# Kernel tuning notes

Measured on AMD Instinct MI355X. Metric: run time of the kernel, lower is better.

## Reference

```python
import jax, jax.numpy as jnp
import numpy as np

D_MODEL = 1024


def setup_inputs() -> dict:
    key = jax.random.key(0)
    k1, k2, k3, k4, k5, k6 = jax.random.split(key, 6)
    B, S, D = 4, 4096, D_MODEL
    scale = 1.0 / np.sqrt(D)
    return {
        "hidden": jax.random.normal(k1, (B, S, D), dtype=jnp.float32),
        "pre_emb": jax.random.normal(k2, (B, S, D), dtype=jnp.float32),
        "w1": jax.random.normal(k3, (D, D), dtype=jnp.float32) * scale,  # [in, out]
        "b1": jax.random.normal(k4, (D,), dtype=jnp.float32) * 0.01,
        "w2": jax.random.normal(k5, (D, D), dtype=jnp.float32) * scale,
        "b2": jax.random.normal(k6, (D,), dtype=jnp.float32) * 0.01,
    }


def reference(hidden, pre_emb, w1, b1, w2, b2):
    # h = Linear1(hidden); i = Linear2(hidden + pre_emb)
    h = jnp.einsum("bsd,de->bse", hidden, w1) + b1            # [B,S,D]
    i = jnp.einsum("bsd,de->bse", hidden + pre_emb, w2) + b2  # [B,S,D]
    attn = jnp.einsum("bqd,bkd->bqk", h, i)                   # [B,S,S]
    return jax.nn.softmax(attn, axis=-1)
```

## Files before the change

### kernel.cpp

```cpp
#include <hip/hip_runtime.h>
#include <hip/hip_bf16.h>
#include <stdint.h>

#define DM   1024
#define BATCH 4
#define SEQ  4096
#define MTOT (BATCH*SEQ)

typedef __attribute__((ext_vector_type(8))) short bf16x8;
typedef __attribute__((ext_vector_type(4))) float f32x4;

#define GLOAD_LDS16(gp, lp) __builtin_amdgcn_global_load_lds( \
    (const __attribute__((address_space(1))) unsigned int*)(gp), \
    (__attribute__((address_space(3))) unsigned int*)(lp), 16, 0, 0)

__device__ __forceinline__ ushort f2bf(float f){
  uint u = __float_as_uint(f);
  u += 0x7FFFu + ((u >> 16) & 1u);
  return (ushort)(u >> 16);
}
__device__ __forceinline__ float bf2f(ushort b){ return __uint_as_float(((uint)b) << 16); }

__device__ __forceinline__ void split4(const float4 v, ushort4& h4, ushort4& l4){
  h4.x = f2bf(v.x); l4.x = f2bf(v.x - bf2f(h4.x));
  h4.y = f2bf(v.y); l4.y = f2bf(v.y - bf2f(h4.y));
  h4.z = f2bf(v.z); l4.z = f2bf(v.z - bf2f(h4.z));
  h4.w = f2bf(v.w); l4.w = f2bf(v.w - bf2f(h4.w));
}

__global__ __launch_bounds__(256)
void prep_w_split(const float* __restrict__ w1, const float* __restrict__ w2,
                  ushort* __restrict__ w1h, ushort* __restrict__ w1l,
                  ushort* __restrict__ w2h, ushort* __restrict__ w2l){
  const float* w = blockIdx.y ? w2 : w1;
  ushort* oh = blockIdx.y ? w2h : w1h;
  ushort* ol = blockIdx.y ? w2l : w1l;
  size_t off = ((size_t)blockIdx.x * 256 + threadIdx.x) * 4;
  float4 v = *(const float4*)&w[off];
  ushort4 h4, l4; split4(v, h4, l4);
  *(ushort4*)&oh[off] = h4;
  *(ushort4*)&ol[off] = l4;
}

__global__ __launch_bounds__(256)
void prep_xy(const float* __restrict__ hidden, const float* __restrict__ pre,
             ushort* __restrict__ xh, ushort* __restrict__ xl,
             ushort* __restrict__ yh, ushort* __restrict__ yl,
             const float* __restrict__ c2, float* __restrict__ beta, int writeX){
  __shared__ float red[4];
  const int tid = threadIdx.x, lane = tid & 63, wid = tid >> 6;
  size_t off = ((size_t)blockIdx.x * 256 + tid) * 4;
  float4 h = *(const float4*)&hidden[off];
  float4 p = *(const float4*)&pre[off];
  float4 y = {h.x + p.x, h.y + p.y, h.z + p.z, h.w + p.w};
  ushort4 a, b;
  if (writeX){
    split4(h, a, b);
    *(ushort4*)&xh[off] = a;
    *(ushort4*)&xl[off] = b;
  }
  split4(y, a, b);
  *(ushort4*)&yh[off] = a;
  *(ushort4*)&yl[off] = b;

  float4 c = *(const float4*)&c2[tid * 4];
  float s = y.x * c.x + y.y * c.y + y.z * c.z + y.w * c.w;
  #pragma unroll
  for (int o = 32; o > 0; o >>= 1) s += __shfl_xor(s, o, 64);
  if (lane == 0) red[wid] = s;
  __syncthreads();
  if (tid == 0) beta[blockIdx.x] = red[0] + red[1] + red[2] + red[3];
}

__global__ __launch_bounds__(256)
void c2k(const float* __restrict__ w2, const float* __restrict__ b1,
         float* __restrict__ c2){
  const int wid = threadIdx.x >> 6, lane = threadIdx.x & 63;
  const int row = blockIdx.x * 4 + wid;
  float s = 0.f;
  #pragma unroll
  for (int t = 0; t < 16; t++){
    int e = lane + 64 * t;
    s += w2[(size_t)row * DM + e] * b1[e];
  }
  #pragma unroll
  for (int o = 32; o > 0; o >>= 1) s += __shfl_xor(s, o, 64);
  if (lane == 0) c2[row] = s;
}

__device__ __forceinline__ void bt_mainloop(
    const ushort* __restrict__ Aph, const ushort* __restrict__ Apl,
    const ushort* __restrict__ Bph, const ushort* __restrict__ Bpl,
    int m0, int n0, f32x4 (&acc)[4][4]){
  __shared__ alignas(16) ushort Ah[128*32];
  __shared__ alignas(16) ushort Al[128*32];
  __shared__ alignas(16) ushort Bh[128*32];
  __shared__ alignas(16) ushort Bl[128*32];

  const int tid = threadIdx.x;
  const int lane = tid & 63, wid = tid >> 6;
  const int wm = (wid & 1) * 64, wn = (wid >> 1) * 64;
  const int lr = lane & 15;
  const int lks = (((lane >> 4) ^ ((lane >> 1) & 3)) << 3);

  const ushort* plane = (wid == 0) ? Aph : (wid == 1) ? Apl : (wid == 2) ? Bph : Bpl;
  ushort* lds = (wid == 0) ? Ah : (wid == 1) ? Al : (wid == 2) ? Bh : Bl;
  const int r0 = (wid < 2) ? m0 : n0;
  const size_t goff = (size_t)(r0 + (lane >> 2)) * DM
                    + (size_t)(((lane & 3) ^ ((lane >> 3) & 3)) * 8);

  for (int k0 = 0; k0 < DM; k0 += 32){
    __syncthreads();
    const ushort* gp = plane + goff + k0;
    #pragma unroll
    for (int t = 0; t < 8; t++){
      GLOAD_LDS16(gp + (size_t)t * 16 * DM, lds + t * 512);
    }
    __syncthreads();

    bf16x8 fah[4], fal[4], fbh[4], fbl[4];
    #pragma unroll
    for (int i = 0; i < 4; i++){
      fah[i] = *(const bf16x8*)&Ah[(wm + i*16 + lr)*32 + lks];
      fal[i] = *(const bf16x8*)&Al[(wm + i*16 + lr)*32 + lks];
      fbh[i] = *(const bf16x8*)&Bh[(wn + i*16 + lr)*32 + lks];
      fbl[i] = *(const bf16x8*)&Bl[(wn + i*16 + lr)*32 + lks];
    }
    #pragma unroll
    for (int i = 0; i < 4; i++)
      #pragma unroll
      for (int j = 0; j < 4; j++){
        acc[i][j] = __builtin_amdgcn_mfma_f32_16x16x32_bf16(fah[i], fbh[j], acc[i][j], 0, 0, 0);
        acc[i][j] = __builtin_amdgcn_mfma_f32_16x16x32_bf16(fah[i], fbl[j], acc[i][j], 0, 0, 0);
        acc[i][j] = __builtin_amdgcn_mfma_f32_16x16x32_bf16(fal[i], fbh[j], acc[i][j], 0, 0, 0);
      }
  }
}

__global__ __launch_bounds__(256, 2)
void gemm_bt_split(const ushort* __restrict__ Aph, const ushort* __restrict__ Apl,
                   const ushort* __restrict__ Bph, const ushort* __restrict__ Bpl,
                   ushort* __restrict__ oh, ushort* __restrict__ ol){
  const int m0 = blockIdx.y * 128, n0 = blockIdx.x * 128;
  f32x4 acc[4][4];
  for (int i = 0; i < 4; i++) for (int j = 0; j < 4; j++) acc[i][j] = (f32x4){0.f,0.f,0.f,0.f};
  bt_mainloop(Aph, Apl, Bph, Bpl, m0, n0, acc);

  const int lane = threadIdx.x & 63, wid = threadIdx.x >> 6;
  const int wm = (wid & 1) * 64, wn = (wid >> 1) * 64;
  const int lr = lane & 15;
  const int rbase = (lane >> 4) * 4;
  #pragma unroll
  for (int i = 0; i < 4; i++)
    #pragma unroll
    for (int j = 0; j < 4; j++){
      int gc = n0 + wn + j*16 + lr;
      #pragma unroll
      for (int r = 0; r < 4; r++){
        int gr = m0 + wm + i*16 + rbase + r;
        float v = acc[i][j][r];
        ushort hb = f2bf(v);
        size_t o = (size_t)gr * DM + gc;
        oh[o] = hb;
        ol[o] = f2bf(v - bf2f(hb));
      }
    }
}

__global__ __launch_bounds__(256, 2)
void gemm_bt_f32(const ushort* __restrict__ Aph, const ushort* __restrict__ Apl,
                 const ushort* __restrict__ Bph, const ushort* __restrict__ Bpl,
                 float* __restrict__ out){
  const int b = blockIdx.y;
  const int id = blockIdx.x;
  const int c = id & 7;
  const int m = (id >> 3) & 63;
  const int s = m >> 3, u = m & 7;
  const int g = id >> 9;
  const int qt = 16*g + 8*(c & 1) + s;
  const int kt = 8*(c >> 1) + u;
  const int m0 = qt * 128, n0 = kt * 128;
  const size_t abase = (size_t)b * SEQ * DM;

  f32x4 acc[4][4];
  for (int i = 0; i < 4; i++) for (int j = 0; j < 4; j++) acc[i][j] = (f32x4){0.f,0.f,0.f,0.f};
  bt_mainloop(Aph + abase, Apl + abase, Bph + abase, Bpl + abase, m0, n0, acc);

  const int lane = threadIdx.x & 63, wid = threadIdx.x >> 6;
  const int wm = (wid & 1) * 64, wn = (wid >> 1) * 64;
  const int lr = lane & 15;
  const int rbase = (lane >> 4) * 4;
  #pragma unroll
  for (int i = 0; i < 4; i++)
    #pragma unroll
    for (int j = 0; j < 4; j++){
      int gc = n0 + wn + j*16 + lr;
      #pragma unroll
      for (int r = 0; r < 4; r++){
        int gr = m0 + wm + i*16 + rbase + r;
        __builtin_nontemporal_store(acc[i][j][r],
            &out[((size_t)b * SEQ + gr) * SEQ + gc]);
      }
    }
}

#define ASTR 40
__global__ __launch_bounds__(256, 2)
void gemm_z_manual(const float* __restrict__ hidden,
                   const ushort* __restrict__ gth, const ushort* __restrict__ gtl,
                   ushort* __restrict__ zh, ushort* __restrict__ zl){
  const int m0 = blockIdx.y * 128, n0 = blockIdx.x * 128;
  __shared__ alignas(16) ushort Ah[128*ASTR];
  __shared__ alignas(16) ushort Al[128*ASTR];
  __shared__ alignas(16) ushort Bh[128*32];
  __shared__ alignas(16) ushort Bl[128*32];

  const int tid = threadIdx.x;
  const int lane = tid & 63, wid = tid >> 6;
  const int wm = (wid & 1) * 64, wn = (wid >> 1) * 64;
  const int lr = lane & 15, lk = (lane >> 4) * 8;
  const int lks = (((lane >> 4) ^ ((lane >> 1) & 3)) << 3);

  const ushort* bp = (wid < 2) ? gth : gtl;
  ushort* blds = (wid < 2) ? Bh : Bl;
  const int tb = (wid & 1) * 4;
  const size_t bgoff = (size_t)(n0 + (lane >> 2)) * DM
                     + (size_t)(((lane & 3) ^ ((lane >> 3) & 3)) * 8);

  f32x4 acc[4][4];
  for (int i = 0; i < 4; i++) for (int j = 0; j < 4; j++) acc[i][j] = (f32x4){0.f,0.f,0.f,0.f};

  for (int k0 = 0; k0 < DM; k0 += 32){
    __syncthreads();
    const ushort* gb = bp + bgoff + k0;
    #pragma unroll
    for (int t = 0; t < 4; t++){
      GLOAD_LDS16(gb + (size_t)(tb + t) * 16 * DM, blds + (tb + t) * 512);
    }
    #pragma unroll
    for (int c = 0; c < 4; c++){
      int idx = c * 256 + tid;
      int row = idx >> 3, kq = (idx & 7) * 4;
      size_t ga = (size_t)(m0 + row) * DM + k0 + kq;
      float4 v = *(const float4*)&hidden[ga];
      ushort4 h4, l4;
      split4(v, h4, l4);
      *(ushort4*)&Ah[row*ASTR + kq] = h4;
      *(ushort4*)&Al[row*ASTR + kq] = l4;
    }
    __syncthreads();

    bf16x8 fah[4], fal[4], fbh[4], fbl[4];
    #pragma unroll
    for (int i = 0; i < 4; i++){
      fah[i] = *(const bf16x8*)&Ah[(wm + i*16 + lr)*ASTR + lk];
      fal[i] = *(const bf16x8*)&Al[(wm + i*16 + lr)*ASTR + lk];
      fbh[i] = *(const bf16x8*)&Bh[(wn + i*16 + lr)*32 + lks];
      fbl[i] = *(const bf16x8*)&Bl[(wn + i*16 + lr)*32 + lks];
    }
    #pragma unroll
    for (int i = 0; i < 4; i++)
      #pragma unroll
      for (int j = 0; j < 4; j++){
        acc[i][j] = __builtin_amdgcn_mfma_f32_16x16x32_bf16(fah[i], fbh[j], acc[i][j], 0, 0, 0);
        acc[i][j] = __builtin_amdgcn_mfma_f32_16x16x32_bf16(fah[i], fbl[j], acc[i][j], 0, 0, 0);
        acc[i][j] = __builtin_amdgcn_mfma_f32_16x16x32_bf16(fal[i], fbh[j], acc[i][j], 0, 0, 0);
      }
  }

  const int rbase = (lane >> 4) * 4;
  #pragma unroll
  for (int i = 0; i < 4; i++)
    #pragma unroll
    for (int j = 0; j < 4; j++){
      int gc = n0 + wn + j*16 + lr;
      #pragma unroll
      for (int r = 0; r < 4; r++){
        int gr = m0 + wm + i*16 + rbase + r;
        float v = acc[i][j][r];
        ushort hb = f2bf(v);
        size_t o = (size_t)gr * DM + gc;
        zh[o] = hb;
        zl[o] = f2bf(v - bf2f(hb));
      }
    }
}

__global__ __launch_bounds__(256)
void softmax_rows(float* __restrict__ out, const float* __restrict__ beta){
  __shared__ float red[8];
  const size_t row = blockIdx.x;
  float* p = out + row * (size_t)SEQ;
  const float* bp = beta + ((row >> 12) << 12);
  const int tid = threadIdx.x, lane = tid & 63, wid = tid >> 6;

  f32x4 v[4];
  float m = -3.0e38f;
  #pragma unroll
  for (int c = 0; c < 4; c++){
    v[c] = __builtin_nontemporal_load(((const f32x4*)p) + c*256 + tid);
    f32x4 bb = *(((const f32x4*)bp) + c*256 + tid);
    v[c] += bb;
    m = fmaxf(m, fmaxf(fmaxf(v[c].x, v[c].y), fmaxf(v[c].z, v[c].w)));
  }
  #pragma unroll
  for (int o = 32; o > 0; o >>= 1) m = fmaxf(m, __shfl_xor(m, o, 64));
  if (lane == 0) red[wid] = m;
  __syncthreads();
  const float M = fmaxf(fmaxf(red[0], red[1]), fmaxf(red[2], red[3]));

  float s = 0.f;
  #pragma unroll
  for (int c = 0; c < 4; c++){
    v[c].x = __expf(v[c].x - M); s += v[c].x;
    v[c].y = __expf(v[c].y - M); s += v[c].y;
    v[c].z = __expf(v[c].z - M); s += v[c].z;
    v[c].w = __expf(v[c].w - M); s += v[c].w;
  }
  #pragma unroll
  for (int o = 32; o > 0; o >>= 1) s += __shfl_xor(s, o, 64);
  if (lane == 0) red[4 + wid] = s;
  __syncthreads();
  const float inv = 1.0f / (red[4] + red[5] + red[6] + red[7]);
  #pragma unroll
  for (int c = 0; c < 4; c++){
    v[c] *= inv;
    __builtin_nontemporal_store(v[c], ((f32x4*)p) + c*256 + tid);
  }
}

extern "C" void kernel_launch(void* const* d_in, const int* in_sizes, int n_in,
                              void* d_out, int out_size, void* d_ws, size_t ws_size,
                              hipStream_t stream){
  const float* hidden = (const float*)d_in[0];
  const float* pre    = (const float*)d_in[1];
  const float* w1     = (const float*)d_in[2];
  const float* b1     = (const float*)d_in[3];
  const float* w2     = (const float*)d_in[4];
  float* out = (float*)d_out;

  char* ws = (char*)d_ws;
  const size_t WP = (size_t)DM * DM * sizeof(ushort);
  const size_t AP = (size_t)MTOT * DM * sizeof(ushort);
  const bool big = ws_size >= 6*AP + 6*WP + (1u << 20);

  ushort *w1h, *w1l, *w2h, *w2l, *Gth, *Gtl, *Xh, *Xl, *Yh, *Yl, *Zh, *Zl;
  float *c2, *beta;
  if (big){
    Xh  = (ushort*)(ws + 0*AP);  Xl  = (ushort*)(ws + 1*AP);
    Yh  = (ushort*)(ws + 2*AP);  Yl  = (ushort*)(ws + 3*AP);
    Zh  = (ushort*)(ws + 4*AP);  Zl  = (ushort*)(ws + 5*AP);
    w1h = (ushort*)(ws + 6*AP);          w1l = (ushort*)(ws + 6*AP + WP);
    w2h = (ushort*)(ws + 6*AP + 2*WP);   w2l = (ushort*)(ws + 6*AP + 3*WP);
    Gth = (ushort*)(ws + 6*AP + 4*WP);   Gtl = (ushort*)(ws + 6*AP + 5*WP);
    c2   = (float*)(ws + 6*AP + 6*WP);
    beta = c2 + DM;
  } else {
    Zh  = (ushort*)(ws + 0*AP);  Zl  = (ushort*)(ws + 1*AP);
    Yh  = (ushort*)(ws + 2*AP);  Yl  = (ushort*)(ws + 3*AP);
    Gth = (ushort*)(ws + 4*AP);  Gtl = (ushort*)(ws + 4*AP + WP);
    w1h = (ushort*)(ws + 0);       w1l = (ushort*)(ws + WP);
    w2h = (ushort*)(ws + 2*WP);    w2l = (ushort*)(ws + 3*WP);
    c2   = (float*)(ws + 4*AP + 2*WP);
    beta = c2 + DM;
    Xh = Xl = nullptr;
  }

  prep_w_split<<<dim3(1024, 2), 256, 0, stream>>>(w1, w2, w1h, w1l, w2h, w2l);
  c2k<<<dim3(256), 256, 0, stream>>>(w2, b1, c2);
  prep_xy<<<dim3(16384), 256, 0, stream>>>(hidden, pre, Xh, Xl, Yh, Yl, c2, beta, big ? 1 : 0);
  gemm_bt_split<<<dim3(8, 8), 256, 0, stream>>>(w2h, w2l, w1h, w1l, Gth, Gtl);
  if (big){
    gemm_bt_split<<<dim3(8, 128), 256, 0, stream>>>(Xh, Xl, Gth, Gtl, Zh, Zl);
  } else {
    gemm_z_manual<<<dim3(8, 128), 256, 0, stream>>>(hidden, Gth, Gtl, Zh, Zl);
  }
  gemm_bt_f32<<<dim3(1024, BATCH), 256, 0, stream>>>(Zh, Zl, Yh, Yl, out);
  softmax_rows<<<dim3(MTOT), 256, 0, stream>>>(out, beta);
}
```

Baseline: 936.3 us.

## Use 256x256 tiles with 8 waves and double-buffered LDS pipeline for split-bf16 GEMMs

Adds a new main loop that computes 256x256 output tiles with 512 threads. It double-buffers LDS and interleaves quarter-tile global-to-LDS loads with the MFMA phases, using explicit vmcnt waits, barriers and setprio. Both the attention-score GEMM and the big-path Z GEMM switch to it, which raises data reuse per load and hides load latency. The cost is more registers and LDS per block, which may limit occupancy, and fewer blocks, which may cause tail effects.

Measured after the change: 866.5 us. 1.08x faster.

```diff
diff --git a/kernel.cpp b/kernel.cpp
--- a/kernel.cpp
+++ b/kernel.cpp
@@ -13,6 +13,10 @@
 #define GLOAD_LDS16(gp, lp) __builtin_amdgcn_global_load_lds( \
     (const __attribute__((address_space(1))) unsigned int*)(gp), \
     (__attribute__((address_space(3))) unsigned int*)(lp), 16, 0, 0)
+
+#define VMCNT(n) asm volatile("s_waitcnt vmcnt(" #n ")" ::: "memory")
+#define BAR()    __builtin_amdgcn_s_barrier()
+#define FENCE()  asm volatile("" ::: "memory")
 
 __device__ __forceinline__ ushort f2bf(float f){
   uint u = __float_as_uint(f);
@@ -88,6 +92,158 @@
   if (lane == 0) c2[row] = s;
 }
 
+__device__ __forceinline__ void mainloop256(
+    const ushort* __restrict__ Aph, const ushort* __restrict__ Apl,
+    const ushort* __restrict__ Bph, const ushort* __restrict__ Bpl,
+    int m0, int n0, f32x4 (&acc)[8][4]){
+  __shared__ alignas(16) ushort lds[2][4][256*32];
+
+  const int tid = threadIdx.x;
+  const int lane = tid & 63, wv = tid >> 6;
+  const int wm = (wv & 1) * 128, wn = (wv >> 1) * 64;
+  const int lr = lane & 15;
+  const int lks = (((lane >> 4) ^ ((lane >> 1) & 3)) << 3);
+
+  const int rowidx = tid >> 2;
+  const int srcc = (((tid & 3) ^ ((tid >> 3) & 3)) << 3);
+  const int arow = rowidx + (rowidx & 64);
+  const int brow = ((rowidx >> 5) << 6) + (rowidx & 31);
+  const int awrow = wv * 16 + ((wv & 4) << 4);
+  const int bwrow = ((wv >> 1) << 6) + ((wv & 1) << 4);
+
+  auto stageA = [&](int bf, int qa, int kt){
+    const size_t g = (size_t)(m0 + qa * 64 + arow) * DM + kt * 32 + srcc;
+    GLOAD_LDS16(Aph + g, &lds[bf][0][(qa * 64 + awrow) * 32]);
+    GLOAD_LDS16(Apl + g, &lds[bf][1][(qa * 64 + awrow) * 32]);
+  };
+  auto stageB = [&](int bf, int qb, int kt){
+    const size_t g = (size_t)(n0 + qb * 32 + brow) * DM + kt * 32 + srcc;
+    GLOAD_LDS16(Bph + g, &lds[bf][2][(qb * 32 + bwrow) * 32]);
+    GLOAD_LDS16(Bpl + g, &lds[bf][3][(qb * 32 + bwrow) * 32]);
+  };
+
+  bf16x8 ah[4], al[4], bh0[2], bl0[2], bh1[2], bl1[2];
+
+#define DS_A(CUR, QA) do { _Pragma("unroll") for (int i = 0; i < 4; i++){ \
+    ah[i] = *(const bf16x8*)&lds[CUR][0][(wm + (QA)*64 + i*16 + lr)*32 + lks]; \
+    al[i] = *(const bf16x8*)&lds[CUR][1][(wm + (QA)*64 + i*16 + lr)*32 + lks]; } } while(0)
+#define DS_B(CUR, QB, BH, BL) do { _Pragma("unroll") for (int j = 0; j < 2; j++){ \
+    BH[j] = *(const bf16x8*)&lds[CUR][2][(wn + (QB)*32 + j*16 + lr)*32 + lks]; \
+    BL[j] = *(const bf16x8*)&lds[CUR][3][(wn + (QB)*32 + j*16 + lr)*32 + lks]; } } while(0)
+#define MFMA3(QA, QB, BH, BL) do { \
+  __builtin_amdgcn_s_setprio(1); \
+  _Pragma("unroll") for (int i = 0; i < 4; i++) _Pragma("unroll") for (int j = 0; j < 2; j++) \
+    acc[(QA)*4+i][(QB)*2+j] = __builtin_amdgcn_mfma_f32_16x16x32_bf16(ah[i], BH[j], acc[(QA)*4+i][(QB)*2+j], 0, 0, 0); \
+  _Pragma("unroll") for (int i = 0; i < 4; i++) _Pragma("unroll") for (int j = 0; j < 2; j++) \
+    acc[(QA)*4+i][(QB)*2+j] = __builtin_amdgcn_mfma_f32_16x16x32_bf16(ah[i], BL[j], acc[(QA)*4+i][(QB)*2+j], 0, 0, 0); \
+  _Pragma("unroll") for (int i = 0; i < 4; i++) _Pragma("unroll") for (int j = 0; j < 2; j++) \
+    acc[(QA)*4+i][(QB)*2+j] = __builtin_amdgcn_mfma_f32_16x16x32_bf16(al[i], BH[j], acc[(QA)*4+i][(QB)*2+j], 0, 0, 0); \
+  __builtin_amdgcn_s_setprio(0); } while(0)
+
+  stageA(0, 0, 0); stageB(0, 0, 0); stageB(0, 1, 0); stageA(0, 1, 0);
+
+  for (int t = 0; t < 31; ++t){
+    const int cur = t & 1, nxt = cur ^ 1;
+    VMCNT(4); BAR(); FENCE();
+    DS_A(cur, 0); DS_B(cur, 0, bh0, bl0);
+    stageA(nxt, 0, t + 1);
+    MFMA3(0, 0, bh0, bl0);
+    BAR();
+    VMCNT(4); BAR(); FENCE();
+    DS_B(cur, 1, bh1, bl1);
+    stageB(nxt, 0, t + 1);
+    MFMA3(0, 1, bh1, bl1);
+    BAR();
+    VMCNT(4); BAR(); FENCE();
+    DS_A(cur, 1);
+    stageB(nxt, 1, t + 1);
+    MFMA3(1, 1, bh1, bl1);
+    BAR();
+    stageA(nxt, 1, t + 1);
+    MFMA3(1, 0, bh0, bl0);
+    BAR();
+  }
+  {
+    VMCNT(4); BAR(); FENCE();
+    DS_A(1, 0); DS_B(1, 0, bh0, bl0);
+    MFMA3(0, 0, bh0, bl0);
+    BAR();
+    VMCNT(2); BAR(); FENCE();
+    DS_B(1, 1, bh1, bl1);
+    MFMA3(0, 1, bh1, bl1);
+    BAR();
+    VMCNT(0); BAR(); FENCE();
+    DS_A(1, 1);
+    MFMA3(1, 1, bh1, bl1);
+    BAR();
+    MFMA3(1, 0, bh0, bl0);
+  }
+#undef DS_A
+#undef DS_B
+#undef MFMA3
+}
+
+__global__ __launch_bounds__(512, 2)
+void gemm_bt_split256(const ushort* __restrict__ Aph, const ushort* __restrict__ Apl,
+                      const ushort* __restrict__ Bph, const ushort* __restrict__ Bpl,
+                      ushort* __restrict__ oh, ushort* __restrict__ ol){
+  const int m0 = blockIdx.y * 256, n0 = blockIdx.x * 256;
+  f32x4 acc[8][4] = {};
+  mainloop256(Aph, Apl, Bph, Bpl, m0, n0, acc);
+
+  const int tid = threadIdx.x, lane = tid & 63, wv = tid >> 6;
+  const int wm = (wv & 1) * 128, wn = (wv >> 1) * 64;
+  const int lr = lane & 15, rbase = (lane >> 4) * 4;
+  #pragma unroll
+  for (int I = 0; I < 8; I++)
+    #pragma unroll
+    for (int J = 0; J < 4; J++){
+      int gc = n0 + wn + J*16 + lr;
+      #pragma unroll
+      for (int r = 0; r < 4; r++){
+        int gr = m0 + wm + I*16 + rbase + r;
+        float v = acc[I][J][r];
+        ushort hb = f2bf(v);
+        size_t o = (size_t)gr * DM + gc;
+        oh[o] = hb;
+        ol[o] = f2bf(v - bf2f(hb));
+      }
+    }
+}
+
+__global__ __launch_bounds__(512, 2)
+void gemm_bt_f32_256(const ushort* __restrict__ Aph, const ushort* __restrict__ Apl,
+                     const ushort* __restrict__ Bph, const ushort* __restrict__ Bpl,
+                     float* __restrict__ out){
+  const int b = blockIdx.y;
+  const int id = blockIdx.x;
+  const int c = id & 7;
+  const int m = id >> 3;
+  const int qt = (c >> 1) * 4 + (m >> 3);
+  const int kt = (c & 1) * 8 + (m & 7);
+  const int m0 = qt * 256, n0 = kt * 256;
+  const size_t abase = (size_t)b * SEQ * DM;
+
+  f32x4 acc[8][4] = {};
+  mainloop256(Aph + abase, Apl + abase, Bph + abase, Bpl + abase, m0, n0, acc);
+
+  const int tid = threadIdx.x, lane = tid & 63, wv = tid >> 6;
+  const int wm = (wv & 1) * 128, wn = (wv >> 1) * 64;
+  const int lr = lane & 15, rbase = (lane >> 4) * 4;
+  #pragma unroll
+  for (int I = 0; I < 8; I++)
+    #pragma unroll
+    for (int J = 0; J < 4; J++){
+      int gc = n0 + wn + J*16 + lr;
+      #pragma unroll
+      for (int r = 0; r < 4; r++){
+        int gr = m0 + wm + I*16 + rbase + r;
+        __builtin_nontemporal_store(acc[I][J][r],
+            &out[((size_t)b * SEQ + gr) * SEQ + gc]);
+      }
+    }
+}
+
 __device__ __forceinline__ void bt_mainloop(
     const ushort* __restrict__ Aph, const ushort* __restrict__ Apl,
     const ushort* __restrict__ Bph, const ushort* __restrict__ Bpl,
@@ -163,43 +319,6 @@
         size_t o = (size_t)gr * DM + gc;
         oh[o] = hb;
         ol[o] = f2bf(v - bf2f(hb));
-      }
-    }
-}
-
-__global__ __launch_bounds__(256, 2)
-void gemm_bt_f32(const ushort* __restrict__ Aph, const ushort* __restrict__ Apl,
-                 const ushort* __restrict__ Bph, const ushort* __restrict__ Bpl,
-                 float* __restrict__ out){
-  const int b = blockIdx.y;
-  const int id = blockIdx.x;
-  const int c = id & 7;
-  const int m = (id >> 3) & 63;
-  const int s = m >> 3, u = m & 7;
-  const int g = id >> 9;
-  const int qt = 16*g + 8*(c & 1) + s;
-  const int kt = 8*(c >> 1) + u;
-  const int m0 = qt * 128, n0 = kt * 128;
-  const size_t abase = (size_t)b * SEQ * DM;
-
-  f32x4 acc[4][4];
-  for (int i = 0; i < 4; i++) for (int j = 0; j < 4; j++) acc[i][j] = (f32x4){0.f,0.f,0.f,0.f};
-  bt_mainloop(Aph + abase, Apl + abase, Bph + abase, Bpl + abase, m0, n0, acc);
-
-  const int lane = threadIdx.x & 63, wid = threadIdx.x >> 6;
-  const int wm = (wid & 1) * 64, wn = (wid >> 1) * 64;
-  const int lr = lane & 15;
-  const int rbase = (lane >> 4) * 4;
-  #pragma unroll
-  for (int i = 0; i < 4; i++)
-    #pragma unroll
-    for (int j = 0; j < 4; j++){
-      int gc = n0 + wn + j*16 + lr;
-      #pragma unroll
-      for (int r = 0; r < 4; r++){
-        int gr = m0 + wm + i*16 + rbase + r;
-        __builtin_nontemporal_store(acc[i][j][r],
-            &out[((size_t)b * SEQ + gr) * SEQ + gc]);
       }
     }
 }
@@ -371,10 +490,10 @@
   prep_xy<<<dim3(16384), 256, 0, stream>>>(hidden, pre, Xh, Xl, Yh, Yl, c2, beta, big ? 1 : 0);
   gemm_bt_split<<<dim3(8, 8), 256, 0, stream>>>(w2h, w2l, w1h, w1l, Gth, Gtl);
   if (big){
-    gemm_bt_split<<<dim3(8, 128), 256, 0, stream>>>(Xh, Xl, Gth, Gtl, Zh, Zl);
+    gemm_bt_split256<<<dim3(4, 64), 512, 0, stream>>>(Xh, Xl, Gth, Gtl, Zh, Zl);
   } else {
     gemm_z_manual<<<dim3(8, 128), 256, 0, stream>>>(hidden, Gth, Gtl, Zh, Zl);
   }
-  gemm_bt_f32<<<dim3(1024, BATCH), 256, 0, stream>>>(Zh, Zl, Yh, Yl, out);
+  gemm_bt_f32_256<<<dim3(256, BATCH), 512, 0, stream>>>(Zh, Zl, Yh, Yl, out);
   softmax_rows<<<dim3(MTOT), 256, 0, stream>>>(out, beta);
 }
```
